# Performance work log

Measured on AMD Instinct MI355X. Metric: run time of the kernel, lower is better.

Reference implementation:

```python
import jax, jax.numpy as jnp
import numpy as np

D_MODEL = 768
NUM_HEADS = 12
D_K = D_MODEL // NUM_HEADS


def setup_inputs() -> dict:
    key = jax.random.key(0)
    ks = jax.random.split(key, 5)
    B, S = 2, 2048
    scale = 1.0 / np.sqrt(D_MODEL)
    return {
        "x": jax.random.normal(ks[0], (B, S, D_MODEL), dtype=jnp.float32),
        "q_proj_weight": jax.random.normal(ks[1], (D_MODEL, D_MODEL), dtype=jnp.float32) * scale,
        "k_proj_weight": jax.random.normal(ks[2], (D_MODEL, D_MODEL), dtype=jnp.float32) * scale,
        "v_proj_weight": jax.random.normal(ks[3], (D_MODEL, D_MODEL), dtype=jnp.float32) * scale,
        "o_proj_weight": jax.random.normal(ks[4], (D_MODEL, D_MODEL), dtype=jnp.float32) * scale,
    }


def reference(x, q_proj_weight, k_proj_weight, v_proj_weight, o_proj_weight):
    B, S, _ = x.shape
    H, dk = NUM_HEADS, D_K
    # projections: weight is [d_out, d_in], applied as x @ W^T
    Q = jnp.einsum("bsd,ed->bse", x, q_proj_weight).reshape(B, S, H, dk)
    K = jnp.einsum("bsd,ed->bse", x, k_proj_weight).reshape(B, S, H, dk)
    V = jnp.einsum("bsd,ed->bse", x, v_proj_weight).reshape(B, S, H, dk)
    # scores [b, h, q, k]
    scores = jnp.einsum("bqhd,bkhd->bhqk", Q, K) / jnp.sqrt(jnp.float32(dk))
    causal = jnp.tril(jnp.ones((S, S), dtype=bool))
    scores = jnp.where(causal, scores, -jnp.inf)
    attn = jax.nn.softmax(scores, axis=-1)
    out = jnp.einsum("bhqk,bkhd->bqhd", attn, V).reshape(B, S, H * dk)
    return jnp.einsum("bsd,ed->bse", out, o_proj_weight)
```

## Files before the change

### kernel.cpp

```cpp
#include <hip/hip_runtime.h>
#include <hip/hip_bf16.h>
#include <stdint.h>

typedef __hip_bfloat16 bf16;
typedef __attribute__((ext_vector_type(8))) short short8;
typedef __attribute__((ext_vector_type(4))) float f32x4;
typedef __attribute__((ext_vector_type(16))) float f32x16;

#define MFMA16(A, B, C) __builtin_amdgcn_mfma_f32_16x16x32_bf16(A, B, C, 0, 0, 0)
#define MFMA32(A, B, C) __builtin_amdgcn_mfma_f32_32x32x16_bf16(A, B, C, 0, 0, 0)

#define SB 2
#define SS 2048
#define SD 768
#define SH 12
#define SM (SB*SS)
#define BHSD (SB*SH*SS*64)
#define QSCALE 0.18033688011112042f

__device__ __forceinline__ void gload_lds16(const bf16* g, bf16* l) {
    __builtin_amdgcn_global_load_lds(
        (const __attribute__((address_space(1))) void*)(g),
        (__attribute__((address_space(3))) void*)(l),
        16, 0, 0);
}

__device__ __forceinline__ int cvtpk(float a, float b) {
    int r;
    asm("v_cvt_pk_bf16_f32 %0, %1, %2" : "=v"(r) : "v"(a), "v"(b));
    return r;
}
__device__ __forceinline__ void plswap(int& a, int& b) {
    asm("v_permlane32_swap_b32 %0, %1" : "+v"(a), "+v"(b));
}

__global__ void cvt_all(const float4* __restrict__ x,  const float4* __restrict__ w0,
                        const float4* __restrict__ w1, const float4* __restrict__ w2,
                        const float4* __restrict__ w3,
                        uint64_t* __restrict__ xb, uint64_t* __restrict__ wqkv,
                        uint64_t* __restrict__ wob) {
    int bid = blockIdx.x;
    const float4* s; uint64_t* d; int base;
    if (bid < 3072) { s = x; d = xb; base = bid << 8; }
    else {
        int t = bid - 3072, seg = t / 576, li = t - seg * 576;
        s = (seg == 0) ? w0 : (seg == 1) ? w1 : (seg == 2) ? w2 : w3;
        d = (seg < 3) ? (wqkv + seg * 147456) : wob;
        base = li << 8;
    }
    int i = base + threadIdx.x;
    float4 v = s[i];
    union { bf16 h[4]; uint64_t u; } p;
    p.h[0] = __float2bfloat16(v.x);
    p.h[1] = __float2bfloat16(v.y);
    p.h[2] = __float2bfloat16(v.z);
    p.h[3] = __float2bfloat16(v.w);
    d[i] = p.u;
}

template<int EPI>
__global__ __launch_bounds__(256) void gemm_bt(const bf16* __restrict__ A,
                                               const bf16* __restrict__ Bw,
                                               void* __restrict__ Out,
                                               int K) {
    __shared__ bf16 lA[128 * 64];
    __shared__ bf16 lB[128 * 64];
    const int tid  = threadIdx.x;
    const int lane = tid & 63;
    const int wid  = tid >> 6;
    const int wr = wid >> 1, wc = wid & 1;
    const int m0 = blockIdx.y * 128, n0 = blockIdx.x * 128;
    const int g = lane >> 4, l15 = lane & 15;
    const int srow = lane >> 3, slot = lane & 7;

    f32x4 acc[4][4] = {};

    for (int kt = 0; kt < K; kt += 64) {
        __syncthreads();
        #pragma unroll
        for (int p = 0; p < 4; ++p) {
            int c = wid * 4 + p;
            int row = c * 8 + srow;
            int colsw = (slot ^ (row & 7)) * 8;
            gload_lds16(A  + (m0 + row) * K + kt + colsw, &lA[c * 512]);
            gload_lds16(Bw + (n0 + row) * K + kt + colsw, &lB[c * 512]);
        }
        __syncthreads();
        #pragma unroll
        for (int ks = 0; ks < 2; ++ks) {
            short8 af[4], bfv[4];
            #pragma unroll
            for (int m = 0; m < 4; ++m) {
                int row = wr * 64 + m * 16 + l15;
                int idx = row * 64 + (((ks * 4 + g) ^ (row & 7)) * 8);
                af[m] = *reinterpret_cast<const short8*>(&lA[idx]);
            }
            #pragma unroll
            for (int n = 0; n < 4; ++n) {
                int row = wc * 64 + n * 16 + l15;
                int idx = row * 64 + (((ks * 4 + g) ^ (row & 7)) * 8);
                bfv[n] = *reinterpret_cast<const short8*>(&lB[idx]);
            }
            #pragma unroll
            for (int m = 0; m < 4; ++m)
                #pragma unroll
                for (int n = 0; n < 4; ++n)
                    acc[m][n] = MFMA16(af[m], bfv[n], acc[m][n]);
        }
    }

    #pragma unroll
    for (int m = 0; m < 4; ++m) {
        #pragma unroll
        for (int n = 0; n < 4; ++n) {
            int col = n0 + wc * 64 + n * 16 + l15;
            #pragma unroll
            for (int r = 0; r < 4; ++r) {
                int row = m0 + wr * 64 + m * 16 + g * 4 + r;
                float v = acc[m][n][r];
                if constexpr (EPI == 0) {
                    int which = (col >= 1536) ? 2 : (col >= 768 ? 1 : 0);
                    int e = col - which * 768;
                    int h = e >> 6, d = e & 63;
                    int b = row >> 11, s = row & 2047;
                    int bh = b * SH + h;
                    bf16* dst = (bf16*)Out;
                    int idx;
                    if (which == 2) idx = 2 * BHSD + (bh * 64 + d) * SS + s;
                    else            idx = which * BHSD + (bh * SS + s) * 64 + d;
                    if (which == 0) v *= QSCALE;
                    dst[idx] = __float2bfloat16(v);
                } else {
                    ((float*)Out)[row * SD + col] = v;
                }
            }
        }
    }
}

__global__ __launch_bounds__(256, 4) void attn_kernel(const bf16* __restrict__ Qb,
                                                      const bf16* __restrict__ Kb,
                                                      const bf16* __restrict__ Vtb,
                                                      float* __restrict__ Op,
                                                      float* __restrict__ lp) {
    __shared__ bf16 lK[2][4096];
    __shared__ bf16 lV[2][4096];

    const int bid = blockIdx.x;
    const int xcd = bid & 7, li = bid >> 3;
    const int g40 = li / 40;
    const int bh = xcd * 3 + g40;
    const int u = 39 - (li - g40 * 40);

    int qg, ck;
    if (u < 4)       { qg = u;                           ck = 0; }
    else if (u < 12) { int t = u - 4;  qg = 4 + (t >> 1);  ck = t & 1; }
    else if (u < 24) { int t = u - 12; int q3 = t / 3; qg = 8 + q3; ck = t - 3 * q3; }
    else             { int t = u - 24; qg = 12 + (t >> 2); ck = t & 3; }

    const int tid = threadIdx.x, lane = tid & 63, w = tid >> 6;
    const int l31 = lane & 31, hi = lane >> 5;
    const int srow = lane >> 3, slot = lane & 7;

    const int j  = qg * 4 + w;
    const int jp = 2 * qg + (w >> 1);
    const int p0 = ck * 8;
    const int pe_ = 2 * qg + 1;
    const int pe = (p0 + 7 < pe_) ? (p0 + 7) : pe_;

    const bf16* Qh = Qb + bh * SS * 64;
    const bf16* Kh = Kb + bh * SS * 64;
    const bf16* Vh = Vtb + bh * 64 * SS;

    const int qself = j * 32 + l31;
    short8 qf[4];
    #pragma unroll
    for (int ks = 0; ks < 4; ++ks)
        qf[ks] = *reinterpret_cast<const short8*>(Qh + qself * 64 + ks * 16 + hi * 8);

    f32x16 oacc[2];
    #pragma unroll
    for (int n = 0; n < 2; ++n)
        #pragma unroll
        for (int r = 0; r < 16; ++r) oacc[n][r] = 0.f;
    float lrow = 0.f;

    auto STAGE = [&](int buf, int kt) {
        #pragma unroll
        for (int p = 0; p < 2; ++p) {
            int c = w * 2 + p;
            int row = c * 8 + srow;
            int colsw = (slot ^ (row & 7)) * 8;
            gload_lds16(Kh + (kt * 64 + row) * 64 + colsw, &lK[buf][c * 512]);
            gload_lds16(Vh + row * SS + kt * 64 + colsw, &lV[buf][c * 512]);
        }
    };

    auto HALF = [&](int cur, int T, int h) {
        f32x16 s_;
        #pragma unroll
        for (int r = 0; r < 16; ++r) s_[r] = 0.f;

        __builtin_amdgcn_s_setprio(1);
        #pragma unroll
        for (int ks = 0; ks < 4; ++ks) {
            int row = h * 32 + l31;
            int idx = row * 64 + (((2 * ks + hi) ^ (row & 7)) * 8);
            short8 kf = *reinterpret_cast<const short8*>(&lK[cur][idx]);
            s_ = MFMA32(kf, qf[ks], s_);
        }
        __builtin_amdgcn_s_setprio(0);

        if (T == j) {
            #pragma unroll
            for (int r = 0; r < 16; ++r) {
                int kvrow = (r & 3) + 8 * (r >> 2) + 4 * hi;
                if (kvrow > l31) s_[r] = -1e30f;
            }
        }

        #pragma unroll
        for (int r = 0; r < 16; ++r) s_[r] = exp2f(s_[r]);
        float w0 = ((s_[0] + s_[1]) + (s_[2] + s_[3]))
                 + ((s_[4] + s_[5]) + (s_[6] + s_[7]));
        float w1 = ((s_[8] + s_[9]) + (s_[10] + s_[11]))
                 + ((s_[12] + s_[13]) + (s_[14] + s_[15]));
        lrow += (w0 + w1);

        int a0 = cvtpk(s_[0],  s_[1]),  a1 = cvtpk(s_[2],  s_[3]);
        int b0 = cvtpk(s_[4],  s_[5]),  b1 = cvtpk(s_[6],  s_[7]);
        plswap(a0, b0); plswap(a1, b1);
        int a2 = cvtpk(s_[8],  s_[9]),  a3 = cvtpk(s_[10], s_[11]);
        int b2 = cvtpk(s_[12], s_[13]), b3 = cvtpk(s_[14], s_[15]);
        plswap(a2, b2); plswap(a3, b3);
        union { int wd[4]; short8 s8; } u0_, u1_;
        u0_.wd[0] = a0; u0_.wd[1] = a1; u0_.wd[2] = b0; u0_.wd[3] = b1;
        u1_.wd[0] = a2; u1_.wd[1] = a3; u1_.wd[2] = b2; u1_.wd[3] = b3;

        __builtin_amdgcn_s_setprio(1);
        #pragma unroll
        for (int n = 0; n < 2; ++n) {
            int rowv = n * 32 + l31;
            int base = rowv * 64;
            int sw = rowv & 7;
            short8 vf0 = *reinterpret_cast<const short8*>(&lV[cur][base + (((4 * h + 0 + hi) ^ sw) * 8)]);
            oacc[n] = MFMA32(u0_.s8, vf0, oacc[n]);
            short8 vf1 = *reinterpret_cast<const short8*>(&lV[cur][base + (((4 * h + 2 + hi) ^ sw) * 8)]);
            oacc[n] = MFMA32(u1_.s8, vf1, oacc[n]);
        }
        __builtin_amdgcn_s_setprio(0);
    };

    STAGE(0, p0);

    int cur = 0;
    for (int pt = p0; pt <= pe; ++pt) {
        if (pt < pe) {
            STAGE(cur ^ 1, pt + 1);
            asm volatile("s_waitcnt vmcnt(4)" ::: "memory");
        } else {
            asm volatile("s_waitcnt vmcnt(0)" ::: "memory");
        }
        __builtin_amdgcn_sched_barrier(0);
        __builtin_amdgcn_s_barrier();
        __builtin_amdgcn_sched_barrier(0);

        if (pt <= jp) {
            const int T0 = 2 * pt, T1 = T0 + 1;
            HALF(cur, T0, 0);
            if (T1 <= j) HALF(cur, T1, 1);
        }

        __builtin_amdgcn_s_barrier();
        cur ^= 1;
    }

    const int qrow0 = bh * SS + j * 32;
    atomicAdd(&lp[qrow0 + l31], lrow);
    #pragma unroll
    for (int n = 0; n < 2; ++n) {
        #pragma unroll
        for (int r = 0; r < 16; ++r) {
            int q = (r & 3) + 8 * (r >> 2) + 4 * hi;
            int d = n * 32 + l31;
            atomicAdd(&Op[(qrow0 + q) * 64 + d], oacc[n][r]);
        }
    }
}

__global__ __launch_bounds__(256) void norm_kernel(const float* __restrict__ Op,
                                                   const float* __restrict__ lp,
                                                   bf16* __restrict__ AO) {
    int idx = blockIdx.x * 256 + threadIdx.x;
    int d = idx & 63, srow = idx >> 6;
    int bh = srow >> 11, s = srow & 2047;
    int b = bh / SH, h = bh - b * SH;
    float v = Op[idx] / lp[srow];
    AO[(b * SS + s) * SD + h * 64 + d] = __float2bfloat16(v);
}

extern "C" void kernel_launch(void* const* d_in, const int* in_sizes, int n_in,
                              void* d_out, int out_size, void* d_ws, size_t ws_size,
                              hipStream_t stream) {
    const float* x  = (const float*)d_in[0];
    const float* wq = (const float*)d_in[1];
    const float* wk = (const float*)d_in[2];
    const float* wv = (const float*)d_in[3];
    const float* wo = (const float*)d_in[4];
    float* out = (float*)d_out;

    bf16* xb   = (bf16*)d_ws;
    bf16* wqkv = xb + SM * SD;
    bf16* wob  = wqkv + 3 * SD * SD;
    bf16* qkv  = wob + SD * SD;
    float* Op  = (float*)(qkv + 3 * BHSD);
    float* lp  = Op + 3145728;
    bf16* ao   = xb;

    hipMemsetAsync(Op, 0, (3145728 + SB * SH * SS) * sizeof(float), stream);

    cvt_all<<<3072 + 4 * 576, 256, 0, stream>>>(
        (const float4*)x, (const float4*)wq, (const float4*)wk,
        (const float4*)wv, (const float4*)wo,
        (uint64_t*)xb, (uint64_t*)wqkv, (uint64_t*)wob);

    gemm_bt<0><<<dim3(2304 / 128, SM / 128), 256, 0, stream>>>(xb, wqkv, (void*)qkv, SD);
    attn_kernel<<<960, 256, 0, stream>>>(qkv, qkv + BHSD, qkv + 2 * BHSD, Op, lp);
    norm_kernel<<<3145728 / 256, 256, 0, stream>>>(Op, lp, ao);
    gemm_bt<1><<<dim3(SD / 128, SM / 128), 256, 0, stream>>>(ao, wob, (void*)out, SD);
}
```

Baseline: 118.3 us.

## Fuse fp32 conversion and softmax normalization into GEMM A-tile loads

The separate x-to-bf16 conversion pass and the norm kernel are removed. Each GEMM now reads fp32 A directly, converts it to bf16 in registers and stores it to LDS. For the output projection it also gathers the per-head attention accumulator and divides by the row sum. The memset becomes a custom zeroing kernel. This cuts two full passes over large intermediates and two launches. In exchange, A loads double in bytes and lose the async global-to-LDS path, and the QKV GEMM reads the fp32 x 18 times across column tiles.

```diff
diff --git a/kernel.cpp b/kernel.cpp
--- a/kernel.cpp
+++ b/kernel.cpp
@@ -34,21 +34,18 @@
     asm("v_permlane32_swap_b32 %0, %1" : "+v"(a), "+v"(b));
 }
 
-__global__ void cvt_all(const float4* __restrict__ x,  const float4* __restrict__ w0,
-                        const float4* __restrict__ w1, const float4* __restrict__ w2,
-                        const float4* __restrict__ w3,
-                        uint64_t* __restrict__ xb, uint64_t* __restrict__ wqkv,
-                        uint64_t* __restrict__ wob) {
+__global__ void zero_ws(float4* __restrict__ p) {
+    p[blockIdx.x * 256 + threadIdx.x] = make_float4(0.f, 0.f, 0.f, 0.f);
+}
+
+__global__ void cvt_w(const float4* __restrict__ w0, const float4* __restrict__ w1,
+                      const float4* __restrict__ w2, const float4* __restrict__ w3,
+                      uint64_t* __restrict__ wqkv, uint64_t* __restrict__ wob) {
     int bid = blockIdx.x;
-    const float4* s; uint64_t* d; int base;
-    if (bid < 3072) { s = x; d = xb; base = bid << 8; }
-    else {
-        int t = bid - 3072, seg = t / 576, li = t - seg * 576;
-        s = (seg == 0) ? w0 : (seg == 1) ? w1 : (seg == 2) ? w2 : w3;
-        d = (seg < 3) ? (wqkv + seg * 147456) : wob;
-        base = li << 8;
-    }
-    int i = base + threadIdx.x;
+    int seg = bid / 576, li = bid - seg * 576;
+    const float4* s = (seg == 0) ? w0 : (seg == 1) ? w1 : (seg == 2) ? w2 : w3;
+    uint64_t* d = (seg < 3) ? (wqkv + seg * 147456) : wob;
+    int i = (li << 8) + threadIdx.x;
     float4 v = s[i];
     union { bf16 h[4]; uint64_t u; } p;
     p.h[0] = __float2bfloat16(v.x);
@@ -58,10 +55,11 @@
     d[i] = p.u;
 }
 
-template<int EPI>
-__global__ __launch_bounds__(256) void gemm_bt(const bf16* __restrict__ A,
+template<int EPI, int ASRC>
+__global__ __launch_bounds__(256) void gemm_bt(const void* __restrict__ Av,
                                                const bf16* __restrict__ Bw,
                                                void* __restrict__ Out,
+                                               const float* __restrict__ lpn,
                                                int K) {
     __shared__ bf16 lA[128 * 64];
     __shared__ bf16 lB[128 * 64];
@@ -82,7 +80,28 @@
             int c = wid * 4 + p;
             int row = c * 8 + srow;
             int colsw = (slot ^ (row & 7)) * 8;
-            gload_lds16(A  + (m0 + row) * K + kt + colsw, &lA[c * 512]);
+            {
+                const float* src;
+                float scale;
+                if constexpr (ASRC == 2) {
+                    int grow = m0 + row;
+                    int b = grow >> 11, s = grow & 2047;
+                    int srowi = (b * SH + (kt >> 6)) * SS + s;
+                    src = (const float*)Av + (size_t)srowi * 64 + colsw;
+                    scale = 1.0f / lpn[srowi];
+                } else {
+                    src = (const float*)Av + (size_t)(m0 + row) * K + kt + colsw;
+                    scale = 1.0f;
+                }
+                float4 v0 = *(const float4*)src;
+                float4 v1 = *(const float4*)(src + 4);
+                union { int wd[4]; short8 s8; } uu;
+                uu.wd[0] = cvtpk(v0.x * scale, v0.y * scale);
+                uu.wd[1] = cvtpk(v0.z * scale, v0.w * scale);
+                uu.wd[2] = cvtpk(v1.x * scale, v1.y * scale);
+                uu.wd[3] = cvtpk(v1.z * scale, v1.w * scale);
+                *reinterpret_cast<short8*>(&lA[c * 512 + lane * 8]) = uu.s8;
+            }
             gload_lds16(Bw + (n0 + row) * K + kt + colsw, &lB[c * 512]);
         }
         __syncthreads();
@@ -288,17 +307,6 @@
     }
 }
 
-__global__ __launch_bounds__(256) void norm_kernel(const float* __restrict__ Op,
-                                                   const float* __restrict__ lp,
-                                                   bf16* __restrict__ AO) {
-    int idx = blockIdx.x * 256 + threadIdx.x;
-    int d = idx & 63, srow = idx >> 6;
-    int bh = srow >> 11, s = srow & 2047;
-    int b = bh / SH, h = bh - b * SH;
-    float v = Op[idx] / lp[srow];
-    AO[(b * SS + s) * SD + h * 64 + d] = __float2bfloat16(v);
-}
-
 extern "C" void kernel_launch(void* const* d_in, const int* in_sizes, int n_in,
                               void* d_out, int out_size, void* d_ws, size_t ws_size,
                               hipStream_t stream) {
@@ -309,23 +317,21 @@
     const float* wo = (const float*)d_in[4];
     float* out = (float*)d_out;
 
-    bf16* xb   = (bf16*)d_ws;
-    bf16* wqkv = xb + SM * SD;
+    bf16* wqkv = (bf16*)d_ws;
     bf16* wob  = wqkv + 3 * SD * SD;
     bf16* qkv  = wob + SD * SD;
     float* Op  = (float*)(qkv + 3 * BHSD);
     float* lp  = Op + 3145728;
-    bf16* ao   = xb;
-
-    hipMemsetAsync(Op, 0, (3145728 + SB * SH * SS) * sizeof(float), stream);
-
-    cvt_all<<<3072 + 4 * 576, 256, 0, stream>>>(
-        (const float4*)x, (const float4*)wq, (const float4*)wk,
-        (const float4*)wv, (const float4*)wo,
-        (uint64_t*)xb, (uint64_t*)wqkv, (uint64_t*)wob);
-
-    gemm_bt<0><<<dim3(2304 / 128, SM / 128), 256, 0, stream>>>(xb, wqkv, (void*)qkv, SD);
+
+    zero_ws<<<3120, 256, 0, stream>>>((float4*)Op);
+
+    cvt_w<<<2304, 256, 0, stream>>>(
+        (const float4*)wq, (const float4*)wk, (const float4*)wv, (const float4*)wo,
+        (uint64_t*)wqkv, (uint64_t*)wob);
+
+    gemm_bt<0, 1><<<dim3(2304 / 128, SM / 128), 256, 0, stream>>>(
+        (const void*)x, wqkv, (void*)qkv, nullptr, SD);
     attn_kernel<<<960, 256, 0, stream>>>(qkv, qkv + BHSD, qkv + 2 * BHSD, Op, lp);
-    norm_kernel<<<3145728 / 256, 256, 0, stream>>>(Op, lp, ao);
-    gemm_bt<1><<<dim3(SD / 128, SM / 128), 256, 0, stream>>>(ao, wob, (void*)out, SD);
-}
+    gemm_bt<1, 2><<<dim3(SD / 128, SM / 128), 256, 0, stream>>>(
+        (const void*)Op, wob, (void*)out, lp, SD);
+}
```

Result: slower. 126.1 us (+6.6%).
